# Performance work log

Hardware: AMD Instinct MI355X
Metric: run time of the kernel (lower is better)

Reference implementation:

```python
import math
import jax, jax.numpy as jnp
import numpy as np

HIDDEN = 2048
N_HEAD = 32
N_KV = 8
HEAD_DIM = HIDDEN // N_HEAD  # 64
B, S = 2, 2048


def setup_inputs() -> dict:
    key = jax.random.key(0)
    ks = jax.random.split(key, 9)
    sc_h = 1.0 / math.sqrt(HIDDEN)
    return {
        "X": jax.random.normal(ks[0], (B, S, HIDDEN), jnp.float32),
        "Wq": jax.random.normal(ks[1], (HIDDEN, HIDDEN), jnp.float32) * sc_h,
        "bq": jax.random.normal(ks[2], (HIDDEN,), jnp.float32) * 0.01,
        "Wk": jax.random.normal(ks[3], (N_KV * HEAD_DIM, HIDDEN), jnp.float32) * sc_h,
        "bk": jax.random.normal(ks[4], (N_KV * HEAD_DIM,), jnp.float32) * 0.01,
        "Wv": jax.random.normal(ks[5], (N_KV * HEAD_DIM, HIDDEN), jnp.float32) * sc_h,
        "bv": jax.random.normal(ks[6], (N_KV * HEAD_DIM,), jnp.float32) * 0.01,
        "Wo": jax.random.normal(ks[7], (HIDDEN, HIDDEN), jnp.float32) * sc_h,
        "bo": jax.random.normal(ks[8], (HIDDEN,), jnp.float32) * 0.01,
    }


def reference(X, Wq, bq, Wk, bk, Wv, bv, Wo, bo):
    b, s, _ = X.shape
    g = N_HEAD // N_KV  # query heads per kv head (repeat_interleave group)
    scale = 1.0 / math.sqrt(HEAD_DIM)

    q = X @ Wq.T + bq                       # [B,S,H*D]
    k = X @ Wk.T + bk                       # [B,S,KV*D]
    v = X @ Wv.T + bv                       # [B,S,KV*D]

    # q grouped as (B, KV, g, S, D): head h = kv*g + j matches repeat_interleave on dim=1
    q = q.reshape(b, s, N_KV, g, HEAD_DIM).transpose(0, 2, 3, 1, 4)  # [B,KV,g,S,D]
    k = k.reshape(b, s, N_KV, HEAD_DIM).transpose(0, 2, 1, 3)         # [B,KV,S,D]
    v = v.reshape(b, s, N_KV, HEAD_DIM).transpose(0, 2, 1, 3)         # [B,KV,S,D]

    # scores without materializing repeated K/V: broadcast kv head over g query heads
    scores = jnp.einsum("bkgqd,bkld->bkgql", q, k) * scale            # [B,KV,g,S,S]
    weights = jax.nn.softmax(scores, axis=-1)
    out = jnp.einsum("bkgql,bkld->bkgqd", weights, v)                 # [B,KV,g,S,D]

    # replicate torch's contiguous .view(B, seq, -1) applied to the [B,H,S,D]
    # tensor WITHOUT transposing back: plain row-major reshape of (B,H,S,D).
    out = out.reshape(b, s, N_HEAD * HEAD_DIM)
    return out @ Wo.T + bo
```

## Files before the change

kernel.cpp:

```cpp
#include <hip/hip_runtime.h>

#define HIDDEN 2048
#define NHEADS 32
#define NKV    8
#define HDIM   64
#define BATCH  2
#define SEQ    2048
#define MROWS  (BATCH*SEQ)
#define NQKV   3072

#define SCALEQ 0.18033688011112042f

typedef _Float16 half8_t __attribute__((ext_vector_type(8)));
typedef _Float16 half4_t __attribute__((ext_vector_type(4)));
typedef __fp16   fp16x2_t __attribute__((ext_vector_type(2)));
typedef float    f32x4_t __attribute__((ext_vector_type(4)));

#define AS1 __attribute__((address_space(1)))
#define AS3 __attribute__((address_space(3)))

__device__ __forceinline__ void async_copy16(void* lds, const void* g) {
    __builtin_amdgcn_global_load_lds((AS1 void*)g, (AS3 void*)lds, 16, 0, 0);
}

#define PRIO1 __builtin_amdgcn_s_setprio(1)
#define PRIO0 __builtin_amdgcn_s_setprio(0)
#define BAR   __builtin_amdgcn_s_barrier()


#define LDA(dst, bi, mh) do {                                                  \
    _Pragma("unroll") for (int mi = 0; mi < 4; ++mi) {                         \
        dst[mi][0] = *(const half8_t*)(&As[bi][abase + (mh)*4096 + mi*1024 + g0]); \
        dst[mi][1] = *(const half8_t*)(&As[bi][abase + (mh)*4096 + mi*1024 + g1]); \
    } } while (0)

#define LDB(dst, bi) do {                                                      \
    _Pragma("unroll") for (int ni = 0; ni < 4; ++ni) {                         \
        dst[ni][0] = *(const half8_t*)(&Bs[bi][bbase + ni*1024 + g0]);         \
        dst[ni][1] = *(const half8_t*)(&Bs[bi][bbase + ni*1024 + g1]);         \
    } } while (0)

#define MFMA_Q(av, bv, mh, nh) do {                                            \
    _Pragma("unroll") for (int mi = 0; mi < 4; ++mi)                           \
    _Pragma("unroll") for (int ni = 0; ni < 2; ++ni) {                         \
        f32x4_t& cc = acc[(mh)*4 + mi][(nh)*2 + ni];                           \
        cc = __builtin_amdgcn_mfma_f32_16x16x32_f16(av[mi][0], bv[(nh)*2+ni][0], cc, 0, 0, 0); \
        cc = __builtin_amdgcn_mfma_f32_16x16x32_f16(av[mi][1], bv[(nh)*2+ni][1], cc, 0, 0, 0); \
    } } while (0)

#define STG_AH(bi, hf, kb) do {                                                \
    async_copy16(&As[bi][(hf)*8192 + ldst],        Ag + (size_t)((hf)*128)      * K + (kb)); \
    async_copy16(&As[bi][(hf)*8192 + 4096 + ldst], Ag + (size_t)((hf)*128 + 64) * K + (kb)); \
  } while (0)
#define STG_BH(bi, hf, kb) do {                                                \
    async_copy16(&Bs[bi][(hf)*8192 + ldst],        Bg + (size_t)((hf)*128)      * K + (kb)); \
    async_copy16(&Bs[bi][(hf)*8192 + 4096 + ldst], Bg + (size_t)((hf)*128 + 64) * K + (kb)); \
  } while (0)

template <typename OutT, bool QKV>
__global__ __launch_bounds__(512, 2) void gemm256(
    const _Float16* __restrict__ A, const _Float16* __restrict__ Bm,
    const float* __restrict__ bias, OutT* __restrict__ C,
    _Float16* __restrict__ kfb, _Float16* __restrict__ vfb,
    int K, int ldc) {
    __shared__ _Float16 As[2][16384];
    __shared__ _Float16 Bs[2][16384];

    const int tid  = threadIdx.x;
    const int wave = tid >> 6;
    const int lane = tid & 63;
    const int quad = lane >> 4;
    const int l16  = lane & 15;
    const int wr   = wave >> 2;
    const int wc   = wave & 3;

    const int nwg = (int)(gridDim.x * gridDim.y);
    const int lin = (int)(blockIdx.y * gridDim.x + blockIdx.x);
    const int q8  = nwg >> 3;
    const int idx = (lin & 7) * q8 + (lin >> 3);
    const int tx  = idx % (int)gridDim.x;
    const int ty  = idx / (int)gridDim.x;
    const int m0  = ty * 256;
    const int n0  = tx * 256;

    const int srow = tid >> 3;
    const int sg   = ((tid & 7) ^ (srow & 7)) << 3;
    const _Float16* Ag = A  + (size_t)(m0 + srow) * K + sg;
    const _Float16* Bg = Bm + (size_t)(n0 + srow) * K + sg;
    const int ldst = wave * 512;

    const int sk = l16 & 7;
    const int g0 = ((0 + quad) ^ sk) << 3;
    const int g1 = ((4 + quad) ^ sk) << 3;
    const int abase = wr * 8192 + l16 * 64;
    const int bbase = wc * 4096 + l16 * 64;

    f32x4_t acc[8][4] = {};

    const int NT    = K >> 6;
    const int iters = NT >> 1;

    STG_AH(0, 0, 0);  STG_AH(0, 1, 0);  STG_BH(0, 0, 0);  STG_BH(0, 1, 0);
    STG_AH(1, 0, 64); STG_AH(1, 1, 64); STG_BH(1, 0, 64); STG_BH(1, 1, 64);
    asm volatile("s_waitcnt vmcnt(8)" ::: "memory");
    BAR;

    for (int i = 0; i < iters; ++i) {
        const int  kb1 = (2 * i + 1) << 6;
        const int  kb2 = (2 * i + 2) << 6;
        const int  kb3 = (2 * i + 3) << 6;
        const bool nx  = (i + 1 < iters);
        half8_t a[4][2], a2[4][2], b[4][2];

        LDA(a, 0, 0);
        LDB(b, 0);
        if (i > 0) STG_AH(1, 1, kb1);
        BAR;
        PRIO1; MFMA_Q(a, b, 0, 0); PRIO0;
        BAR;
        LDA(a2, 0, 1);
        if (nx) STG_BH(0, 0, kb2);
        BAR;
        PRIO1; MFMA_Q(a, b, 0, 1); PRIO0;
        BAR;
        if (nx) STG_BH(0, 1, kb2);
        BAR;
        PRIO1; MFMA_Q(a2, b, 1, 1); PRIO0;
        BAR;
        if (nx) STG_AH(0, 0, kb2);
        BAR;
        PRIO1; MFMA_Q(a2, b, 1, 0); PRIO0;
        if (nx) { asm volatile("s_waitcnt vmcnt(6)" ::: "memory"); }
        else    { asm volatile("s_waitcnt vmcnt(0)" ::: "memory"); }
        BAR;

        LDA(a, 1, 0);
        LDB(b, 1);
        if (nx) STG_AH(0, 1, kb2);
        BAR;
        PRIO1; MFMA_Q(a, b, 0, 0); PRIO0;
        BAR;
        LDA(a2, 1, 1);
        if (nx) STG_BH(1, 0, kb3);
        BAR;
        PRIO1; MFMA_Q(a, b, 0, 1); PRIO0;
        BAR;
        if (nx) STG_BH(1, 1, kb3);
        BAR;
        PRIO1; MFMA_Q(a2, b, 1, 1); PRIO0;
        BAR;
        if (nx) STG_AH(1, 0, kb3);
        BAR;
        PRIO1; MFMA_Q(a2, b, 1, 0); PRIO0;
        if (nx) { asm volatile("s_waitcnt vmcnt(6)" ::: "memory"); }
        else    { asm volatile("s_waitcnt vmcnt(0)" ::: "memory"); }
        BAR;
    }

    if (QKV && n0 >= 2560) {
#pragma unroll
        for (int ni = 0; ni < 4; ++ni) {
            const int c  = n0 + wc * 64 + ni * 16 + l16;
            const int kd = c - 2560;
            const int kv = kd >> 6, d = kd & 63;
            const int dt = (d >> 4) & 3;
            const float bv = bias[c];
#pragma unroll
            for (int mi = 0; mi < 8; ++mi) {
                const int r0   = m0 + wr * 128 + mi * 16 + quad * 4;
                const int bb   = r0 >> 11;
                const int sblk = (r0 & 2047) >> 6;
                const int nt   = (r0 >> 4) & 3;
                half4_t h;
#pragma unroll
                for (int i = 0; i < 4; ++i) h[i] = (_Float16)(acc[mi][ni][i] + bv);
                *(half4_t*)(vfb + ((size_t)(bb * 8 + kv) * 32 + sblk) * 4096 +
                            ((nt * 4 + dt) * 64 + quad * 16 + (d & 15)) * 4) = h;
            }
        }
    } else if (QKV && n0 >= 2048) {
#pragma unroll
        for (int ni = 0; ni < 4; ++ni) {
            const int c  = n0 + wc * 64 + ni * 16 + l16;
            const int kd = c - 2048;
            const int kv = kd >> 6, d = kd & 63;
            const float bv = bias[c];
#pragma unroll
            for (int mi = 0; mi < 8; ++mi) {
                const int r0   = m0 + wr * 128 + mi * 16 + quad * 4;
                const int bb   = r0 >> 11;
                const int sblk = (r0 & 2047) >> 6;
                const int nt   = (r0 >> 4) & 3;
                _Float16* dst = kfb + ((size_t)(bb * 8 + kv) * 32 + sblk) * 4096 +
                    ((nt * 2 + (d >> 5)) * 64 + ((d >> 3) & 3) * 16 + quad * 4) * 8 +
                    (d & 7);
#pragma unroll
                for (int i = 0; i < 4; ++i)
                    dst[i * 8] = (_Float16)(acc[mi][ni][i] + bv);
            }
        }
    } else {
#pragma unroll
        for (int ni = 0; ni < 4; ++ni) {
            const int c  = n0 + wc * 64 + ni * 16 + l16;
            const float bv = bias[c];
#pragma unroll
            for (int mi = 0; mi < 8; ++mi) {
                const int r0 = m0 + wr * 128 + mi * 16 + quad * 4;
#pragma unroll
                for (int i = 0; i < 4; ++i)
                    C[(size_t)(r0 + i) * ldc + c] = (OutT)(acc[mi][ni][i] + bv);
            }
        }
    }
}

__global__ __launch_bounds__(256, 2) void attn_kernel(
    const _Float16* __restrict__ Qb, const _Float16* __restrict__ Kf,
    const _Float16* __restrict__ Vf, _Float16* __restrict__ ctx) {
    __shared__ _Float16 Ks[2][4096];
    __shared__ _Float16 Vs[2][4096];

    const int tid  = threadIdx.x;
    const int wave = tid >> 6;
    const int lane = tid & 63;
    const int quad = lane >> 4;
    const int l16  = lane & 15;
    const int qt  = blockIdx.x;
    const int bkv = blockIdx.y;
    const int b   = bkv >> 3;
    const int kv  = bkv & 7;
    const int h   = kv * 4 + wave;

    half8_t qa[4][2];
#pragma unroll
    for (int g = 0; g < 4; ++g) {
        const _Float16* qp = Qb + ((size_t)(b * SEQ + qt * 64 + g * 16 + l16)) * HIDDEN
                              + h * 64 + quad * 8;
        qa[g][0] = *(const half8_t*)qp;
        qa[g][1] = *(const half8_t*)(qp + 32);
    }

    f32x4_t ot[4][4] = {};
    f32x4_t lacc[4] = {};
    const half4_t ones = {(_Float16)1.f, (_Float16)1.f, (_Float16)1.f, (_Float16)1.f};

    const size_t kvbase = (size_t)(b * 8 + kv) * 32 * 4096;
    const int sh = (wave * 2) * 512 + lane * 8;

#pragma unroll
    for (int j = 0; j < 2; ++j) {
        async_copy16(&Ks[0][(wave * 2 + j) * 512], Kf + kvbase + sh + j * 512);
        async_copy16(&Vs[0][(wave * 2 + j) * 512], Vf + kvbase + sh + j * 512);
    }

    for (int kt = 0; kt < SEQ / 64; ++kt) {
        __syncthreads();
        const int cur = kt & 1;
        if (kt + 1 < SEQ / 64) {
            const int nxt = cur ^ 1;
            const size_t off = kvbase + (size_t)(kt + 1) * 4096 + sh;
#pragma unroll
            for (int j = 0; j < 2; ++j) {
                async_copy16(&Ks[nxt][(wave * 2 + j) * 512], Kf + off + j * 512);
                async_copy16(&Vs[nxt][(wave * 2 + j) * 512], Vf + off + j * 512);
            }
        }

        half8_t kf[4][2];
#pragma unroll
        for (int nt = 0; nt < 4; ++nt) {
#pragma unroll
            for (int c = 0; c < 2; ++c)
                kf[nt][c] = *(const half8_t*)(&Ks[cur][((nt * 2 + c) * 64 + lane) * 8]);
        }

        half4_t p[4][4];
#pragma unroll
        for (int g = 0; g < 4; ++g) {
#pragma unroll
            for (int nt = 0; nt < 4; ++nt) {
                f32x4_t s = {};
                s = __builtin_amdgcn_mfma_f32_16x16x32_f16(kf[nt][0], qa[g][0], s, 0, 0, 0);
                s = __builtin_amdgcn_mfma_f32_16x16x32_f16(kf[nt][1], qa[g][1], s, 0, 0, 0);
                const fp16x2_t lo = __builtin_amdgcn_cvt_pkrtz(
                    __builtin_amdgcn_exp2f(s[0]), __builtin_amdgcn_exp2f(s[1]));
                const fp16x2_t hi = __builtin_amdgcn_cvt_pkrtz(
                    __builtin_amdgcn_exp2f(s[2]), __builtin_amdgcn_exp2f(s[3]));
                half4_t pv;
                pv[0] = (_Float16)lo[0]; pv[1] = (_Float16)lo[1];
                pv[2] = (_Float16)hi[0]; pv[3] = (_Float16)hi[1];
                p[g][nt] = pv;
                lacc[g] = __builtin_amdgcn_mfma_f32_16x16x16f16(ones, pv, lacc[g], 0, 0, 0);
            }
        }

#pragma unroll
        for (int nt = 0; nt < 4; ++nt) {
#pragma unroll
            for (int dt = 0; dt < 4; ++dt) {
                const half4_t vf = *(const half4_t*)(&Vs[cur][((nt * 4 + dt) * 64 + lane) * 4]);
#pragma unroll
                for (int g = 0; g < 4; ++g)
                    ot[g][dt] = __builtin_amdgcn_mfma_f32_16x16x16f16(
                        vf, p[g][nt], ot[g][dt], 0, 0, 0);
            }
        }
    }

    __syncthreads();
    _Float16* T = &Ks[0][0] + wave * 1152;
#pragma unroll
    for (int g = 0; g < 4; ++g) {
        const float inv = 1.f / lacc[g][0];
#pragma unroll
        for (int dt = 0; dt < 4; ++dt) {
            half4_t hh;
#pragma unroll
            for (int r = 0; r < 4; ++r) hh[r] = (_Float16)(ot[g][dt][r] * inv);
            *(half4_t*)(T + l16 * 72 + dt * 16 + quad * 4) = hh;
        }
        __builtin_amdgcn_s_waitcnt(0);
        _Float16* cp = ctx + (((size_t)b * 32 + h) * SEQ + qt * 64 + g * 16 + l16) * 64;
#pragma unroll
        for (int pass = 0; pass < 2; ++pass) {
            const half8_t row = *(const half8_t*)(T + l16 * 72 + pass * 32 + quad * 8);
            *(half8_t*)(cp + pass * 32 + quad * 8) = row;
        }
        __builtin_amdgcn_s_waitcnt(0);
    }
}

__device__ __forceinline__ void cast4(const float* __restrict__ s,
                                      _Float16* __restrict__ d, int i, float sc) {
    const f32x4_t v = ((const f32x4_t*)s)[i];
    half4_t h;
#pragma unroll
    for (int j = 0; j < 4; ++j) h[j] = (_Float16)(v[j] * sc);
    ((half4_t*)d)[i] = h;
}

__global__ __launch_bounds__(256) void prep(
    const float* __restrict__ X,  const float* __restrict__ Wq,
    const float* __restrict__ Wk, const float* __restrict__ Wv,
    const float* __restrict__ Wo, const float* __restrict__ bq,
    const float* __restrict__ bk, const float* __restrict__ bv,
    _Float16* __restrict__ Xh, _Float16* __restrict__ Wqkv,
    _Float16* __restrict__ Woh, float* __restrict__ bqkv) {
    const int bid = blockIdx.x, tid = threadIdx.x;
    if (bid < 8192)       cast4(X,  Xh,   bid * 256 + tid, 1.f);
    else if (bid < 12288) cast4(Wq, Wqkv, (bid - 8192) * 256 + tid, SCALEQ);
    else if (bid < 13312) cast4(Wk, Wqkv + (size_t)HIDDEN * HIDDEN, (bid - 12288) * 256 + tid, 1.f);
    else if (bid < 14336) cast4(Wv, Wqkv + (size_t)(HIDDEN + 512) * HIDDEN, (bid - 13312) * 256 + tid, 1.f);
    else if (bid < 18432) cast4(Wo, Woh,  (bid - 14336) * 256 + tid, 1.f);
    else {
        const int i = (bid - 18432) * 256 + tid;
        if (i < 2048)      bqkv[i] = bq[i] * SCALEQ;
        else if (i < 2560) bqkv[i] = bk[i - 2048];
        else if (i < 3072) bqkv[i] = bv[i - 2560];
    }
}

extern "C" void kernel_launch(void* const* d_in, const int* in_sizes, int n_in,
                              void* d_out, int out_size, void* d_ws, size_t ws_size,
                              hipStream_t stream) {
    const float* X  = (const float*)d_in[0];
    const float* Wq = (const float*)d_in[1];
    const float* bq = (const float*)d_in[2];
    const float* Wk = (const float*)d_in[3];
    const float* bk = (const float*)d_in[4];
    const float* Wv = (const float*)d_in[5];
    const float* bv = (const float*)d_in[6];
    const float* Wo = (const float*)d_in[7];
    const float* bo = (const float*)d_in[8];
    float* out = (float*)d_out;

    char* p = (char*)d_ws;
    _Float16* Xh   = (_Float16*)p; p += (size_t)MROWS * HIDDEN * 2;
    _Float16* Wqkv = (_Float16*)p; p += (size_t)NQKV * HIDDEN * 2;
    _Float16* Woh  = (_Float16*)p; p += (size_t)HIDDEN * HIDDEN * 2;
    float*    bqkv = (float*)p;    p += (size_t)NQKV * 4;
    _Float16* Qb   = (_Float16*)p; p += (size_t)MROWS * HIDDEN * 2;
    _Float16* Kfb  = (_Float16*)p; p += (size_t)16 * 32 * 4096 * 2;
    _Float16* Vfb  = (_Float16*)p; p += (size_t)16 * 32 * 4096 * 2;
    _Float16* ctx  = Xh;

    prep<<<18444, 256, 0, stream>>>(X, Wq, Wk, Wv, Wo, bq, bk, bv,
                                    Xh, Wqkv, Woh, bqkv);

    gemm256<_Float16, true><<<dim3(NQKV / 256, MROWS / 256), 512, 0, stream>>>(
        Xh, Wqkv, bqkv, Qb, Kfb, Vfb, HIDDEN, HIDDEN);

    attn_kernel<<<dim3(SEQ / 64, BATCH * NKV), 256, 0, stream>>>(Qb, Kfb, Vfb, ctx);

    gemm256<float, false><<<dim3(HIDDEN / 256, MROWS / 256), 512, 0, stream>>>(
        ctx, Woh, bo, out, nullptr, nullptr, HIDDEN, HIDDEN);
}
```

Baseline: 348.0 us.

## Shrink GEMM tile to 128x256 and split attention queries across 8 waves

The GEMM moves from 256x256 to 128x256 output tiles. Its pipeline is simplified to one K-tile per iteration, with A staged one step ahead and B two steps ahead, and accumulator registers are halved. The attention kernel now uses 512 threads, so each wave handles 32 query rows instead of 64, and K/V staging uses a single shared buffer. This aims for more workgroups, better CU fill and higher occupancy, at the cost of more global B traffic per output and more per-block overhead.

```diff
diff --git a/kernel.cpp b/kernel.cpp
--- a/kernel.cpp
+++ b/kernel.cpp
@@ -28,42 +28,38 @@
 #define BAR   __builtin_amdgcn_s_barrier()
 
 
-#define LDA(dst, bi, mh) do {                                                  \
-    _Pragma("unroll") for (int mi = 0; mi < 4; ++mi) {                         \
-        dst[mi][0] = *(const half8_t*)(&As[bi][abase + (mh)*4096 + mi*1024 + g0]); \
-        dst[mi][1] = *(const half8_t*)(&As[bi][abase + (mh)*4096 + mi*1024 + g1]); \
+#define STG_A(bi, u, kb) \
+    async_copy16(&As[bi][(u)*4096 + ldst], Ag + (size_t)((u)*64) * K + (kb))
+#define STG_B(bi, u, kb) \
+    async_copy16(&Bs[bi][(u)*4096 + ldst], Bg + (size_t)((u)*64) * K + (kb))
+
+#define LDA2(dst, bi, mh) do {                                                 \
+    _Pragma("unroll") for (int mi = 0; mi < 2; ++mi) {                         \
+        dst[mi][0] = *(const half8_t*)(&As[bi][abase + ((mh)*2+mi)*1024 + g0]);\
+        dst[mi][1] = *(const half8_t*)(&As[bi][abase + ((mh)*2+mi)*1024 + g1]);\
     } } while (0)
 
-#define LDB(dst, bi) do {                                                      \
+#define LDB4(dst, bi) do {                                                     \
     _Pragma("unroll") for (int ni = 0; ni < 4; ++ni) {                         \
         dst[ni][0] = *(const half8_t*)(&Bs[bi][bbase + ni*1024 + g0]);         \
         dst[ni][1] = *(const half8_t*)(&Bs[bi][bbase + ni*1024 + g1]);         \
     } } while (0)
 
-#define MFMA_Q(av, bv, mh, nh) do {                                            \
-    _Pragma("unroll") for (int mi = 0; mi < 4; ++mi)                           \
-    _Pragma("unroll") for (int ni = 0; ni < 2; ++ni) {                         \
-        f32x4_t& cc = acc[(mh)*4 + mi][(nh)*2 + ni];                           \
-        cc = __builtin_amdgcn_mfma_f32_16x16x32_f16(av[mi][0], bv[(nh)*2+ni][0], cc, 0, 0, 0); \
-        cc = __builtin_amdgcn_mfma_f32_16x16x32_f16(av[mi][1], bv[(nh)*2+ni][1], cc, 0, 0, 0); \
+#define MFMA_H(av, mh) do {                                                    \
+    _Pragma("unroll") for (int mi = 0; mi < 2; ++mi)                           \
+    _Pragma("unroll") for (int ni = 0; ni < 4; ++ni) {                         \
+        f32x4_t& cc = acc[(mh)*2 + mi][ni];                                    \
+        cc = __builtin_amdgcn_mfma_f32_16x16x32_f16(av[mi][0], b[ni][0], cc, 0, 0, 0); \
+        cc = __builtin_amdgcn_mfma_f32_16x16x32_f16(av[mi][1], b[ni][1], cc, 0, 0, 0); \
     } } while (0)
 
-#define STG_AH(bi, hf, kb) do {                                                \
-    async_copy16(&As[bi][(hf)*8192 + ldst],        Ag + (size_t)((hf)*128)      * K + (kb)); \
-    async_copy16(&As[bi][(hf)*8192 + 4096 + ldst], Ag + (size_t)((hf)*128 + 64) * K + (kb)); \
-  } while (0)
-#define STG_BH(bi, hf, kb) do {                                                \
-    async_copy16(&Bs[bi][(hf)*8192 + ldst],        Bg + (size_t)((hf)*128)      * K + (kb)); \
-    async_copy16(&Bs[bi][(hf)*8192 + 4096 + ldst], Bg + (size_t)((hf)*128 + 64) * K + (kb)); \
-  } while (0)
-
 template <typename OutT, bool QKV>
-__global__ __launch_bounds__(512, 2) void gemm256(
+__global__ __launch_bounds__(512, 2) void gemm128(
     const _Float16* __restrict__ A, const _Float16* __restrict__ Bm,
     const float* __restrict__ bias, OutT* __restrict__ C,
     _Float16* __restrict__ kfb, _Float16* __restrict__ vfb,
     int K, int ldc) {
-    __shared__ _Float16 As[2][16384];
+    __shared__ _Float16 As[2][8192];
     __shared__ _Float16 Bs[2][16384];
 
     const int tid  = threadIdx.x;
@@ -80,7 +76,7 @@
     const int idx = (lin & 7) * q8 + (lin >> 3);
     const int tx  = idx % (int)gridDim.x;
     const int ty  = idx / (int)gridDim.x;
-    const int m0  = ty * 256;
+    const int m0  = ty * 128;
     const int n0  = tx * 256;
 
     const int srow = tid >> 3;
@@ -92,67 +88,38 @@
     const int sk = l16 & 7;
     const int g0 = ((0 + quad) ^ sk) << 3;
     const int g1 = ((4 + quad) ^ sk) << 3;
-    const int abase = wr * 8192 + l16 * 64;
+    const int abase = wr * 4096 + l16 * 64;
     const int bbase = wc * 4096 + l16 * 64;
 
-    f32x4_t acc[8][4] = {};
-
-    const int NT    = K >> 6;
-    const int iters = NT >> 1;
-
-    STG_AH(0, 0, 0);  STG_AH(0, 1, 0);  STG_BH(0, 0, 0);  STG_BH(0, 1, 0);
-    STG_AH(1, 0, 64); STG_AH(1, 1, 64); STG_BH(1, 0, 64); STG_BH(1, 1, 64);
-    asm volatile("s_waitcnt vmcnt(8)" ::: "memory");
+    f32x4_t acc[4][4] = {};
+    const int NT = K >> 6;
+
+    STG_A(0, 0, 0);  STG_A(0, 1, 0);
+    STG_B(0, 0, 0);  STG_B(0, 1, 0);  STG_B(0, 2, 0);  STG_B(0, 3, 0);
+    STG_B(1, 0, 64); STG_B(1, 1, 64); STG_B(1, 2, 64); STG_B(1, 3, 64);
+    asm volatile("s_waitcnt vmcnt(4)" ::: "memory");
     BAR;
 
-    for (int i = 0; i < iters; ++i) {
-        const int  kb1 = (2 * i + 1) << 6;
-        const int  kb2 = (2 * i + 2) << 6;
-        const int  kb3 = (2 * i + 3) << 6;
-        const bool nx  = (i + 1 < iters);
-        half8_t a[4][2], a2[4][2], b[4][2];
-
-        LDA(a, 0, 0);
-        LDB(b, 0);
-        if (i > 0) STG_AH(1, 1, kb1);
+    for (int t = 0; t < NT; ++t) {
+        const int  cur = t & 1;
+        const int  kA  = (t + 1) << 6;
+        const int  kB  = (t + 2) << 6;
+        const bool sA  = (t + 1 < NT);
+        const bool sB  = (t + 2 < NT);
+        half8_t aL[2][2], aH[2][2], b[4][2];
+
+        LDA2(aL, cur, 0);
+        LDB4(b, cur);
+        if (sA) { STG_A(cur ^ 1, 0, kA); STG_A(cur ^ 1, 1, kA); }
         BAR;
-        PRIO1; MFMA_Q(a, b, 0, 0); PRIO0;
+        PRIO1; MFMA_H(aL, 0); PRIO0;
         BAR;
-        LDA(a2, 0, 1);
-        if (nx) STG_BH(0, 0, kb2);
+        LDA2(aH, cur, 1);
+        if (sB) { STG_B(cur, 0, kB); STG_B(cur, 1, kB);
+                  STG_B(cur, 2, kB); STG_B(cur, 3, kB); }
         BAR;
-        PRIO1; MFMA_Q(a, b, 0, 1); PRIO0;
-        BAR;
-        if (nx) STG_BH(0, 1, kb2);
-        BAR;
-        PRIO1; MFMA_Q(a2, b, 1, 1); PRIO0;
-        BAR;
-        if (nx) STG_AH(0, 0, kb2);
-        BAR;
-        PRIO1; MFMA_Q(a2, b, 1, 0); PRIO0;
-        if (nx) { asm volatile("s_waitcnt vmcnt(6)" ::: "memory"); }
-        else    { asm volatile("s_waitcnt vmcnt(0)" ::: "memory"); }
-        BAR;
-
-        LDA(a, 1, 0);
-        LDB(b, 1);
-        if (nx) STG_AH(0, 1, kb2);
-        BAR;
-        PRIO1; MFMA_Q(a, b, 0, 0); PRIO0;
-        BAR;
-        LDA(a2, 1, 1);
-        if (nx) STG_BH(1, 0, kb3);
-        BAR;
-        PRIO1; MFMA_Q(a, b, 0, 1); PRIO0;
-        BAR;
-        if (nx) STG_BH(1, 1, kb3);
-        BAR;
-        PRIO1; MFMA_Q(a2, b, 1, 1); PRIO0;
-        BAR;
-        if (nx) STG_AH(1, 0, kb3);
-        BAR;
-        PRIO1; MFMA_Q(a2, b, 1, 0); PRIO0;
-        if (nx) { asm volatile("s_waitcnt vmcnt(6)" ::: "memory"); }
+        PRIO1; MFMA_H(aH, 1); PRIO0;
+        if (sB) { asm volatile("s_waitcnt vmcnt(4)" ::: "memory"); }
         else    { asm volatile("s_waitcnt vmcnt(0)" ::: "memory"); }
         BAR;
     }
@@ -166,8 +133,8 @@
             const int dt = (d >> 4) & 3;
             const float bv = bias[c];
 #pragma unroll
-            for (int mi = 0; mi < 8; ++mi) {
-                const int r0   = m0 + wr * 128 + mi * 16 + quad * 4;
+            for (int mi = 0; mi < 4; ++mi) {
+                const int r0   = m0 + wr * 64 + mi * 16 + quad * 4;
                 const int bb   = r0 >> 11;
                 const int sblk = (r0 & 2047) >> 6;
                 const int nt   = (r0 >> 4) & 3;
@@ -186,8 +153,8 @@
             const int kv = kd >> 6, d = kd & 63;
             const float bv = bias[c];
 #pragma unroll
-            for (int mi = 0; mi < 8; ++mi) {
-                const int r0   = m0 + wr * 128 + mi * 16 + quad * 4;
+            for (int mi = 0; mi < 4; ++mi) {
+                const int r0   = m0 + wr * 64 + mi * 16 + quad * 4;
                 const int bb   = r0 >> 11;
                 const int sblk = (r0 & 2047) >> 6;
                 const int nt   = (r0 >> 4) & 3;
@@ -205,8 +172,8 @@
             const int c  = n0 + wc * 64 + ni * 16 + l16;
             const float bv = bias[c];
 #pragma unroll
-            for (int mi = 0; mi < 8; ++mi) {
-                const int r0 = m0 + wr * 128 + mi * 16 + quad * 4;
+            for (int mi = 0; mi < 4; ++mi) {
+                const int r0 = m0 + wr * 64 + mi * 16 + quad * 4;
 #pragma unroll
                 for (int i = 0; i < 4; ++i)
                     C[(size_t)(r0 + i) * ldc + c] = (OutT)(acc[mi][ni][i] + bv);
@@ -215,74 +182,64 @@
     }
 }
 
-__global__ __launch_bounds__(256, 2) void attn_kernel(
+__global__ __launch_bounds__(512, 4) void attn_kernel(
     const _Float16* __restrict__ Qb, const _Float16* __restrict__ Kf,
     const _Float16* __restrict__ Vf, _Float16* __restrict__ ctx) {
-    __shared__ _Float16 Ks[2][4096];
-    __shared__ _Float16 Vs[2][4096];
+    __shared__ _Float16 S[16384];
 
     const int tid  = threadIdx.x;
     const int wave = tid >> 6;
     const int lane = tid & 63;
     const int quad = lane >> 4;
     const int l16  = lane & 15;
+    const int qs   = wave >> 2;
+    const int wh   = wave & 3;
     const int qt  = blockIdx.x;
     const int bkv = blockIdx.y;
     const int b   = bkv >> 3;
     const int kv  = bkv & 7;
-    const int h   = kv * 4 + wave;
-
-    half8_t qa[4][2];
-#pragma unroll
-    for (int g = 0; g < 4; ++g) {
-        const _Float16* qp = Qb + ((size_t)(b * SEQ + qt * 64 + g * 16 + l16)) * HIDDEN
-                              + h * 64 + quad * 8;
+    const int h   = kv * 4 + wh;
+
+    half8_t qa[2][2];
+#pragma unroll
+    for (int g = 0; g < 2; ++g) {
+        const _Float16* qp = Qb +
+            ((size_t)(b * SEQ + qt * 64 + qs * 32 + g * 16 + l16)) * HIDDEN +
+            h * 64 + quad * 8;
         qa[g][0] = *(const half8_t*)qp;
         qa[g][1] = *(const half8_t*)(qp + 32);
     }
 
-    f32x4_t ot[4][4] = {};
-    f32x4_t lacc[4] = {};
+    f32x4_t ot[2][4] = {};
+    f32x4_t lacc[2] = {};
     const half4_t ones = {(_Float16)1.f, (_Float16)1.f, (_Float16)1.f, (_Float16)1.f};
 
     const size_t kvbase = (size_t)(b * 8 + kv) * 32 * 4096;
-    const int sh = (wave * 2) * 512 + lane * 8;
-
-#pragma unroll
-    for (int j = 0; j < 2; ++j) {
-        async_copy16(&Ks[0][(wave * 2 + j) * 512], Kf + kvbase + sh + j * 512);
-        async_copy16(&Vs[0][(wave * 2 + j) * 512], Vf + kvbase + sh + j * 512);
-    }
+    const int sh = wave * 512 + lane * 8;
+
+    async_copy16(&S[wave * 512],        Kf + kvbase + sh);
+    async_copy16(&S[8192 + wave * 512], Vf + kvbase + sh);
 
     for (int kt = 0; kt < SEQ / 64; ++kt) {
         __syncthreads();
         const int cur = kt & 1;
         if (kt + 1 < SEQ / 64) {
-            const int nxt = cur ^ 1;
             const size_t off = kvbase + (size_t)(kt + 1) * 4096 + sh;
-#pragma unroll
-            for (int j = 0; j < 2; ++j) {
-                async_copy16(&Ks[nxt][(wave * 2 + j) * 512], Kf + off + j * 512);
-                async_copy16(&Vs[nxt][(wave * 2 + j) * 512], Vf + off + j * 512);
-            }
-        }
-
-        half8_t kf[4][2];
+            async_copy16(&S[(cur ^ 1) * 4096 + wave * 512],        Kf + off);
+            async_copy16(&S[8192 + (cur ^ 1) * 4096 + wave * 512], Vf + off);
+        }
+        const int kb = cur * 4096, vb = 8192 + cur * 4096;
+
 #pragma unroll
         for (int nt = 0; nt < 4; ++nt) {
-#pragma unroll
-            for (int c = 0; c < 2; ++c)
-                kf[nt][c] = *(const half8_t*)(&Ks[cur][((nt * 2 + c) * 64 + lane) * 8]);
-        }
-
-        half4_t p[4][4];
-#pragma unroll
-        for (int g = 0; g < 4; ++g) {
-#pragma unroll
-            for (int nt = 0; nt < 4; ++nt) {
+            const half8_t kf0 = *(const half8_t*)(&S[kb + ((nt * 2 + 0) * 64 + lane) * 8]);
+            const half8_t kf1 = *(const half8_t*)(&S[kb + ((nt * 2 + 1) * 64 + lane) * 8]);
+            half4_t p[2];
+#pragma unroll
+            for (int g = 0; g < 2; ++g) {
                 f32x4_t s = {};
-                s = __builtin_amdgcn_mfma_f32_16x16x32_f16(kf[nt][0], qa[g][0], s, 0, 0, 0);
-                s = __builtin_amdgcn_mfma_f32_16x16x32_f16(kf[nt][1], qa[g][1], s, 0, 0, 0);
+                s = __builtin_amdgcn_mfma_f32_16x16x32_f16(kf0, qa[g][0], s, 0, 0, 0);
+                s = __builtin_amdgcn_mfma_f32_16x16x32_f16(kf1, qa[g][1], s, 0, 0, 0);
                 const fp16x2_t lo = __builtin_amdgcn_cvt_pkrtz(
                     __builtin_amdgcn_exp2f(s[0]), __builtin_amdgcn_exp2f(s[1]));
                 const fp16x2_t hi = __builtin_amdgcn_cvt_pkrtz(
@@ -290,28 +247,22 @@
                 half4_t pv;
                 pv[0] = (_Float16)lo[0]; pv[1] = (_Float16)lo[1];
                 pv[2] = (_Float16)hi[0]; pv[3] = (_Float16)hi[1];
-                p[g][nt] = pv;
+                p[g] = pv;
                 lacc[g] = __builtin_amdgcn_mfma_f32_16x16x16f16(ones, pv, lacc[g], 0, 0, 0);
             }
-        }
-
-#pragma unroll
-        for (int nt = 0; nt < 4; ++nt) {
 #pragma unroll
             for (int dt = 0; dt < 4; ++dt) {
-                const half4_t vf = *(const half4_t*)(&Vs[cur][((nt * 4 + dt) * 64 + lane) * 4]);
-#pragma unroll
-                for (int g = 0; g < 4; ++g)
-                    ot[g][dt] = __builtin_amdgcn_mfma_f32_16x16x16f16(
-                        vf, p[g][nt], ot[g][dt], 0, 0, 0);
+                const half4_t vf = *(const half4_t*)(&S[vb + ((nt * 4 + dt) * 64 + lane) * 4]);
+                ot[0][dt] = __builtin_amdgcn_mfma_f32_16x16x16f16(vf, p[0], ot[0][dt], 0, 0, 0);
+                ot[1][dt] = __builtin_amdgcn_mfma_f32_16x16x16f16(vf, p[1], ot[1][dt], 0, 0, 0);
             }
         }
     }
 
     __syncthreads();
-    _Float16* T = &Ks[0][0] + wave * 1152;
-#pragma unroll
-    for (int g = 0; g < 4; ++g) {
+    _Float16* T = S + wave * 1152;
+#pragma unroll
+    for (int g = 0; g < 2; ++g) {
         const float inv = 1.f / lacc[g][0];
 #pragma unroll
         for (int dt = 0; dt < 4; ++dt) {
@@ -321,7 +272,8 @@
             *(half4_t*)(T + l16 * 72 + dt * 16 + quad * 4) = hh;
         }
         __builtin_amdgcn_s_waitcnt(0);
-        _Float16* cp = ctx + (((size_t)b * 32 + h) * SEQ + qt * 64 + g * 16 + l16) * 64;
+        _Float16* cp = ctx +
+            (((size_t)b * 32 + h) * SEQ + qt * 64 + qs * 32 + g * 16 + l16) * 64;
 #pragma unroll
         for (int pass = 0; pass < 2; ++pass) {
             const half8_t row = *(const half8_t*)(T + l16 * 72 + pass * 32 + quad * 8);
@@ -388,11 +340,11 @@
     prep<<<18444, 256, 0, stream>>>(X, Wq, Wk, Wv, Wo, bq, bk, bv,
                                     Xh, Wqkv, Woh, bqkv);
 
-    gemm256<_Float16, true><<<dim3(NQKV / 256, MROWS / 256), 512, 0, stream>>>(
+    gemm128<_Float16, true><<<dim3(NQKV / 256, MROWS / 128), 512, 0, stream>>>(
         Xh, Wqkv, bqkv, Qb, Kfb, Vfb, HIDDEN, HIDDEN);
 
-    attn_kernel<<<dim3(SEQ / 64, BATCH * NKV), 256, 0, stream>>>(Qb, Kfb, Vfb, ctx);
-
-    gemm256<float, false><<<dim3(HIDDEN / 256, MROWS / 256), 512, 0, stream>>>(
+    attn_kernel<<<dim3(SEQ / 64, BATCH * NKV), 512, 0, stream>>>(Qb, Kfb, Vfb, ctx);
+
+    gemm128<float, false><<<dim3(HIDDEN / 256, MROWS / 128), 512, 0, stream>>>(
         ctx, Woh, bo, out, nullptr, nullptr, HIDDEN, HIDDEN);
 }
```

New measurement: 320.9 us. -7.8%, faster.
